# Performance work log

Hardware: AMD Instinct MI355X
Metric: run time of the kernel (lower is better)

Reference implementation:

```python
import jax, jax.numpy as jnp
import numpy as np

N = 1_000_000   # total atoms in batched graph
G = 50_000      # number of molecules (graphs)
F = 128         # gnn_out_feats (node feature dim)
H = 128         # classifier_hidden_feats
T = 12          # n_tasks
EPS = 1e-5      # BatchNorm1d eps


def setup_inputs() -> dict:
    key = jax.random.key(0)
    ks = jax.random.split(key, 20)
    s = 0.05
    inp = {}
    inp["node_feats"] = jax.random.normal(ks[0], (N, F), jnp.float32)
    inp["segment_ids"] = jnp.sort(jax.random.randint(ks[1], (N,), 0, G))
    inp["num_graphs"] = G
    # per-task atom weighting: Linear(F,1) per task, stacked -> [T,F]
    inp["atom_w"] = jax.random.normal(ks[2], (T, F), jnp.float32) * s
    inp["atom_b"] = jnp.zeros((T,), jnp.float32)
    # fc_layer 1: Linear(F,H) -> ReLU -> BatchNorm1d(H) (eval mode)
    inp["W1"] = jax.random.normal(ks[3], (T, F, H), jnp.float32) * s
    inp["b1"] = jnp.zeros((T, H), jnp.float32)
    inp["g1"] = jnp.ones((T, H), jnp.float32)
    inp["be1"] = jnp.zeros((T, H), jnp.float32)
    inp["rm1"] = jnp.zeros((T, H), jnp.float32)
    inp["rv1"] = jnp.ones((T, H), jnp.float32)
    # fc_layer 2 and 3: Linear(H,H) -> ReLU -> BatchNorm1d(H)
    inp["W2"] = jax.random.normal(ks[4], (T, H, H), jnp.float32) * s
    inp["b2"] = jnp.zeros((T, H), jnp.float32)
    inp["g2"] = jnp.ones((T, H), jnp.float32)
    inp["be2"] = jnp.zeros((T, H), jnp.float32)
    inp["rm2"] = jnp.zeros((T, H), jnp.float32)
    inp["rv2"] = jnp.ones((T, H), jnp.float32)
    inp["W3"] = jax.random.normal(ks[5], (T, H, H), jnp.float32) * s
    inp["b3"] = jnp.zeros((T, H), jnp.float32)
    inp["g3"] = jnp.ones((T, H), jnp.float32)
    inp["be3"] = jnp.zeros((T, H), jnp.float32)
    inp["rm3"] = jnp.zeros((T, H), jnp.float32)
    inp["rv3"] = jnp.ones((T, H), jnp.float32)
    # output_layer: Linear(H,H) -> ReLU -> Linear(H,1)
    inp["oW1"] = jax.random.normal(ks[6], (T, H, H), jnp.float32) * s
    inp["ob1"] = jnp.zeros((T, H), jnp.float32)
    inp["oW2"] = jax.random.normal(ks[7], (T, H), jnp.float32) * s
    inp["ob2"] = jnp.zeros((T,), jnp.float32)
    return inp


def _fc(x, W, b, g, be, rm, rv):
    # Linear -> ReLU -> BatchNorm1d (eval, running stats), batched over tasks t
    y = jax.nn.relu(jnp.einsum('gti,tio->gto', x, W) + b)
    return (y - rm) * (g * jax.lax.rsqrt(rv + EPS)) + be


def reference(node_feats, segment_ids, num_graphs, atom_w, atom_b,
              W1, b1, g1, be1, rm1, rv1,
              W2, b2, g2, be2, rm2, rv2,
              W3, b3, g3, be3, rm3, rv3,
              oW1, ob1, oW2, ob2):
    n_tasks = atom_w.shape[0]
    # WeightAndSum: per-task sigmoid node weights [N,T]
    w = jax.nn.sigmoid(node_feats @ atom_w.T + atom_b)
    # per-task weighted segment-sum pooling: loop over small fixed task count
    sums = [jax.ops.segment_sum(node_feats * w[:, t:t + 1], segment_ids,
                                num_segments=num_graphs)
            for t in range(n_tasks)]
    mol = jnp.stack(sums, axis=1)  # [G, T, F]
    h = _fc(mol, W1, b1, g1, be1, rm1, rv1)
    h = _fc(h, W2, b2, g2, be2, rm2, rv2)
    h = _fc(h, W3, b3, g3, be3, rm3, rv3)
    z = jax.nn.relu(jnp.einsum('gth,tho->gto', h, oW1) + ob1)
    pred = jnp.einsum('gth,th->gt', z, oW2) + ob2  # [G, T]
    return pred
```

## Files before the change

kernel.cpp:

```cpp
#include <hip/hip_runtime.h>
#include <hip/hip_bf16.h>
#include <hip/hip_fp16.h>

typedef _Float16 f16;
typedef _Float16 f16x2 __attribute__((ext_vector_type(2)));
typedef _Float16 f16x4 __attribute__((ext_vector_type(4)));
typedef _Float16 f16x8 __attribute__((ext_vector_type(8)));
typedef float f32x4 __attribute__((ext_vector_type(4)));

#define BN_EPS 1e-5f

__global__ void seg_starts_k(const int* __restrict__ seg, int N, int G, int* __restrict__ start) {
    int n = blockIdx.x * blockDim.x + threadIdx.x;
    if (n >= N) return;
    int s = seg[n];
    int p = (n == 0) ? -1 : seg[n - 1];
    for (int g = p + 1; g <= s; ++g) start[g] = n;
    if (n == N - 1) {
        for (int g = s + 1; g <= G; ++g) start[g] = N;
    }
}

__global__ void prep_k(const float* __restrict__ W1, const float* __restrict__ b1,
                       const float* __restrict__ W2, const float* __restrict__ b2,
                       const float* __restrict__ W3, const float* __restrict__ b3,
                       const float* __restrict__ oW1, const float* __restrict__ ob1,
                       const float* __restrict__ g1, const float* __restrict__ be1,
                       const float* __restrict__ rm1, const float* __restrict__ rv1,
                       const float* __restrict__ g2, const float* __restrict__ be2,
                       const float* __restrict__ rm2, const float* __restrict__ rv2,
                       const float* __restrict__ g3, const float* __restrict__ be3,
                       const float* __restrict__ rm3, const float* __restrict__ rv3,
                       f16* __restrict__ Wt, float* __restrict__ bp) {
    int T = gridDim.x;
    int t = blockIdx.x, l = blockIdx.y;
    int o = threadIdx.x;
    __shared__ float s_sh[128], c_sh[128];

    const float *W, *b, *gg = nullptr, *be = nullptr, *rm = nullptr, *rv = nullptr;
    if (l == 0)      { W = W1;  b = b1; }
    else if (l == 1) { W = W2;  b = b2;  gg = g1; be = be1; rm = rm1; rv = rv1; }
    else if (l == 2) { W = W3;  b = b3;  gg = g2; be = be2; rm = rm2; rv = rv2; }
    else             { W = oW1; b = ob1; gg = g3; be = be3; rm = rm3; rv = rv3; }

    float s = 1.f, c = 0.f;
    if (gg) {
        float sv = gg[t * 128 + o] * rsqrtf(rv[t * 128 + o] + BN_EPS);
        s = sv;
        c = be[t * 128 + o] - rm[t * 128 + o] * sv;
    }
    s_sh[o] = s;
    c_sh[o] = c;
    __syncthreads();

    const float* Wsrc = W + (size_t)t * 128 * 128;
    f16* Wdst = Wt + (((size_t)l * T + t) * 128 + o) * 128;
    float acc = b[t * 128 + o];
    for (int i = 0; i < 128; ++i) {
        float wv = Wsrc[i * 128 + o];
        Wdst[i] = (f16)(s_sh[i] * wv);
        acc += c_sh[i] * wv;
    }
    bp[((size_t)l * T + t) * 128 + o] = acc;
}

__global__ __launch_bounds__(256) void pool_k(const float* __restrict__ feats,
                                              const float* __restrict__ atom_w,
                                              const float* __restrict__ atom_b,
                                              const int* __restrict__ start,
                                              f16* __restrict__ mol, int G) {
    __shared__ f16 xs_all[4][2][16][128];

    int wave = threadIdx.x >> 6;
    int lane = threadIdx.x & 63;
    f16 (*xs)[16][128] = xs_all[wave];

    int g = blockIdx.x * 4 + wave;
    if (g >= G) return;

    int lr = lane & 15;
    int kg = lane >> 4;

    f16x8 bfr[4];
    float ab = 0.f;
#pragma unroll
    for (int ks = 0; ks < 4; ++ks) {
        f16x8 v = {};
        if (lr < 12) {
            const float* s = atom_w + lr * 128 + ks * 32 + kg * 8;
#pragma unroll
            for (int j = 0; j < 8; ++j) v[j] = (f16)s[j];
        }
        bfr[ks] = v;
    }
    if (lr < 12) ab = atom_b[lr];

    f32x4 acc[8];
#pragma unroll
    for (int nf = 0; nf < 8; ++nf) acc[nf] = (f32x4){0.f, 0.f, 0.f, 0.f};

    int a0 = start[g], a1 = start[g + 1];
    int nAtoms = a1 - a0;
    int nc = (nAtoms + 15) >> 4;

    float4 u[8];
    if (nc > 0) {
        int cn = nAtoms < 16 ? nAtoms : 16;
#pragma unroll
        for (int it = 0; it < 8; ++it) {
            int c = (it << 6) + lane;
            int r = c >> 5, q = c & 31;
            float4 v = make_float4(0.f, 0.f, 0.f, 0.f);
            if (r < cn) v = *(const float4*)(feats + (size_t)(a0 + r) * 128 + (q << 2));
            u[it] = v;
        }
    }

    for (int ci = 0; ci < nc; ++ci) {
        int cur = ci & 1;
#pragma unroll
        for (int it = 0; it < 8; ++it) {
            int c = (it << 6) + lane;
            int r = c >> 5, q = c & 31;
            f16x4 h;
            h[0] = (f16)u[it].x; h[1] = (f16)u[it].y;
            h[2] = (f16)u[it].z; h[3] = (f16)u[it].w;
            *(f16x4*)(&xs[cur][r][(((q >> 1) ^ (r & 7)) << 3) + ((q & 1) << 2)]) = h;
        }
        if (ci + 1 < nc) {
            int c0 = a0 + (ci + 1) * 16;
            int cn2 = a1 - c0; if (cn2 > 16) cn2 = 16;
#pragma unroll
            for (int it = 0; it < 8; ++it) {
                int c = (it << 6) + lane;
                int r = c >> 5, q = c & 31;
                float4 v = make_float4(0.f, 0.f, 0.f, 0.f);
                if (r < cn2) v = *(const float4*)(feats + (size_t)(c0 + r) * 128 + (q << 2));
                u[it] = v;
            }
        }
        int cn = nAtoms - ci * 16; if (cn > 16) cn = 16;

        f32x4 pa = {0.f, 0.f, 0.f, 0.f};
#pragma unroll
        for (int ks = 0; ks < 4; ++ks) {
            f16x8 afr = *(const f16x8*)(&xs[cur][lr][((((ks << 2) + kg)) ^ (lr & 7)) << 3]);
            pa = __builtin_amdgcn_mfma_f32_16x16x32_f16(afr, bfr[ks], pa, 0, 0, 0);
        }
        f16x4 a2;
#pragma unroll
        for (int j = 0; j < 4; ++j) {
            float w = 1.f / (1.f + __expf(-(pa[j] + ab)));
            int atom = (kg << 2) + j;
            a2[j] = (atom < cn) ? (f16)w : (f16)0.f;
        }
#pragma unroll
        for (int nf = 0; nf < 8; ++nf) {
            f16x4 b2;
#pragma unroll
            for (int j = 0; j < 4; ++j) {
                int a = (kg << 2) + j;
                int f = (nf << 4) + lr;
                b2[j] = xs[cur][a][(((f >> 3) ^ (a & 7)) << 3) + (f & 7)];
            }
            acc[nf] = __builtin_amdgcn_mfma_f32_16x16x16f16(a2, b2, acc[nf], 0, 0, 0);
        }
    }

    f16* dst = mol + (size_t)g * 12 * 128;
    if (kg < 3) {
#pragma unroll
        for (int nf = 0; nf < 8; ++nf) {
#pragma unroll
            for (int j = 0; j < 4; ++j) {
                dst[((kg << 2) + j) * 128 + (nf << 4) + lr] = (f16)acc[nf][j];
            }
        }
    }
}

__global__ __launch_bounds__(256, 2) void fc_k(const f16* __restrict__ mol,
                                               const f16* __restrict__ Wt,
                                               const float* __restrict__ bp,
                                               const float* __restrict__ oW2,
                                               const float* __restrict__ ob2,
                                               float* __restrict__ out, int G, int T) {
    __shared__ f16 A[2][64][128];
    __shared__ f16 B[128][128];

    int t = blockIdx.y;
    int g0 = blockIdx.x * 64;
    int tid = threadIdx.x;

    {
#pragma unroll
        for (int k = 0; k < 4; ++k) {
            int c = tid + k * 256;
            int r = c >> 4, sl = c & 15;
            uint4 v = make_uint4(0u, 0u, 0u, 0u);
            if (g0 + r < G)
                v = *(const uint4*)(mol + ((size_t)(g0 + r) * T + t) * 128 + sl * 8);
            *(uint4*)(&A[0][r][(sl ^ (r & 7)) * 8]) = v;
        }
    }
    {
        const f16* src = Wt + ((size_t)0 * T + t) * 128 * 128;
#pragma unroll
        for (int k = 0; k < 8; ++k) {
            int c = tid + k * 256;
            int r = c >> 4, sl = c & 15;
            uint4 v = *(const uint4*)(src + (size_t)r * 128 + sl * 8);
            *(uint4*)(&B[r][(sl ^ (r & 7)) * 8]) = v;
        }
    }
    __syncthreads();

    int wid = tid >> 6, lane = tid & 63;
    int lg = lane >> 4, lr = lane & 15;
    int m0 = wid * 16;
    int arow = m0 + lr;
    float pred[4] = {0.f, 0.f, 0.f, 0.f};
    int cur = 0;

    for (int l = 0; l < 4; ++l) {
        f16x8 afr[4];
#pragma unroll
        for (int ks = 0; ks < 4; ++ks) {
            int sl = (4 * ks + lg) ^ (arow & 7);
            afr[ks] = *(const f16x8*)(&A[cur][arow][sl * 8]);
        }
        const float* bias = bp + ((size_t)l * T + t) * 128;
#pragma unroll
        for (int nf = 0; nf < 8; ++nf) {
            int n = nf * 16 + lr;
            f32x4 acc = {0.f, 0.f, 0.f, 0.f};
#pragma unroll
            for (int ks = 0; ks < 4; ++ks) {
                int sl = (4 * ks + lg) ^ (n & 7);
                f16x8 bfr = *(const f16x8*)(&B[n][sl * 8]);
                acc = __builtin_amdgcn_mfma_f32_16x16x32_f16(afr[ks], bfr, acc, 0, 0, 0);
            }
            float bv = bias[n];
            if (l < 3) {
#pragma unroll
                for (int j = 0; j < 4; ++j) {
                    float y = acc[j] + bv;
                    y = y > 0.f ? y : 0.f;
                    int rr = m0 + 4 * lg + j;
                    A[cur ^ 1][rr][(((n >> 3) ^ (rr & 7)) << 3) + (n & 7)] = (f16)y;
                }
            } else {
                float w2 = oW2[t * 128 + n];
#pragma unroll
                for (int j = 0; j < 4; ++j) {
                    float z = acc[j] + bv;
                    z = z > 0.f ? z : 0.f;
                    pred[j] += z * w2;
                }
            }
        }
        __syncthreads();
        if (l < 3) {
            const f16* src = Wt + ((size_t)(l + 1) * T + t) * 128 * 128;
#pragma unroll
            for (int k = 0; k < 8; ++k) {
                int c = tid + k * 256;
                int r = c >> 4, sl = c & 15;
                uint4 v = *(const uint4*)(src + (size_t)r * 128 + sl * 8);
                *(uint4*)(&B[r][(sl ^ (r & 7)) * 8]) = v;
            }
            __syncthreads();
            cur ^= 1;
        }
    }

#pragma unroll
    for (int m = 1; m < 16; m <<= 1) {
#pragma unroll
        for (int j = 0; j < 4; ++j) pred[j] += __shfl_xor(pred[j], m, 64);
    }
    if (lr == 0) {
        float ob = ob2[t];
#pragma unroll
        for (int j = 0; j < 4; ++j) {
            int gg = g0 + m0 + 4 * lg + j;
            if (gg < G) out[(size_t)gg * T + t] = pred[j] + ob;
        }
    }
}

extern "C" void kernel_launch(void* const* d_in, const int* in_sizes, int n_in,
                              void* d_out, int out_size, void* d_ws, size_t ws_size,
                              hipStream_t stream) {
    const float* node_feats = (const float*)d_in[0];
    const int*   seg        = (const int*)d_in[1];
    const float* atom_w     = (const float*)d_in[3];
    const float* atom_b     = (const float*)d_in[4];
    const float* W1  = (const float*)d_in[5];
    const float* b1  = (const float*)d_in[6];
    const float* g1  = (const float*)d_in[7];
    const float* be1 = (const float*)d_in[8];
    const float* rm1 = (const float*)d_in[9];
    const float* rv1 = (const float*)d_in[10];
    const float* W2  = (const float*)d_in[11];
    const float* b2  = (const float*)d_in[12];
    const float* g2  = (const float*)d_in[13];
    const float* be2 = (const float*)d_in[14];
    const float* rm2 = (const float*)d_in[15];
    const float* rv2 = (const float*)d_in[16];
    const float* W3  = (const float*)d_in[17];
    const float* b3  = (const float*)d_in[18];
    const float* g3  = (const float*)d_in[19];
    const float* be3 = (const float*)d_in[20];
    const float* rm3 = (const float*)d_in[21];
    const float* rv3 = (const float*)d_in[22];
    const float* oW1 = (const float*)d_in[23];
    const float* ob1 = (const float*)d_in[24];
    const float* oW2 = (const float*)d_in[25];
    const float* ob2 = (const float*)d_in[26];

    int T = in_sizes[4];
    int F = in_sizes[3] / T;
    int N = in_sizes[0] / F;
    int G = out_size / T;

    char* ws = (char*)d_ws;
    size_t off = 0;
    int* start = (int*)ws;
    off += (((size_t)(G + 1) * 4) + 255) & ~(size_t)255;
    f16* Wt = (f16*)(ws + off);
    off += (((size_t)4 * T * 128 * 128 * 2) + 255) & ~(size_t)255;
    float* bp = (float*)(ws + off);
    off += (((size_t)4 * T * 128 * 4) + 255) & ~(size_t)255;
    f16* mol = (f16*)(ws + off);

    seg_starts_k<<<(N + 255) / 256, 256, 0, stream>>>(seg, N, G, start);
    prep_k<<<dim3(T, 4), 128, 0, stream>>>(W1, b1, W2, b2, W3, b3, oW1, ob1,
                                           g1, be1, rm1, rv1,
                                           g2, be2, rm2, rv2,
                                           g3, be3, rm3, rv3, Wt, bp);
    pool_k<<<(G + 3) / 4, 256, 0, stream>>>(node_feats, atom_w, atom_b, start, mol, G);
    fc_k<<<dim3((G + 63) / 64, T), 256, 0, stream>>>(mol, Wt, bp, oW2, ob2,
                                                     (float*)d_out, G, T);
}
```

Baseline: 372.6 us.

## Pool over contiguous 128-atom tiles with boundary partials and fixup kernel

Replaces the per-graph, one-wave-per-molecule pooling with blocks that each own a contiguous tile of 128 atoms. Each block computes the sigmoid task weights for the whole tile once, then segment-sums every graph that overlaps the tile. Graphs cut at a tile boundary write fp32 partials to a workspace, and a new fixup kernel adds the two halves. This is meant to remove the padding waste of 16-atom chunks on small graphs and the load imbalance between graphs, and to make feature loads fully coalesced. The cost is an extra launch and partial-sum traffic, and the code assumes no graph spans more than two tiles.

Measured after the change: 424.0 us. 13.8% more time.

```diff
diff --git a/kernel.cpp b/kernel.cpp
--- a/kernel.cpp
+++ b/kernel.cpp
@@ -64,22 +64,27 @@
     bp[((size_t)l * T + t) * 128 + o] = acc;
 }
 
-__global__ __launch_bounds__(256) void pool_k(const float* __restrict__ feats,
-                                              const float* __restrict__ atom_w,
-                                              const float* __restrict__ atom_b,
-                                              const int* __restrict__ start,
-                                              f16* __restrict__ mol, int G) {
-    __shared__ f16 xs_all[4][2][16][128];
-
-    int wave = threadIdx.x >> 6;
-    int lane = threadIdx.x & 63;
-    f16 (*xs)[16][128] = xs_all[wave];
-
-    int g = blockIdx.x * 4 + wave;
-    if (g >= G) return;
-
-    int lr = lane & 15;
-    int kg = lane >> 4;
+__global__ __launch_bounds__(256) void pool2_k(const float* __restrict__ feats,
+                                               const float* __restrict__ atom_w,
+                                               const float* __restrict__ atom_b,
+                                               const int* __restrict__ seg,
+                                               const int* __restrict__ start,
+                                               f16* __restrict__ mol,
+                                               float* __restrict__ pt,
+                                               int N, int G) {
+    __shared__ f16 xs[128][128];
+    __shared__ f16 wls[128][20];
+
+    int b = blockIdx.x;
+    int A0 = b * 128;
+    int cnt = N - A0; if (cnt > 128) cnt = 128;
+    int tid = threadIdx.x;
+    int wave = tid >> 6, lane = tid & 63;
+    int lr = lane & 15, kg = lane >> 4;
+
+    int segPrev = (A0 > 0) ? seg[A0 - 1] : -1;
+    int segFirst = seg[A0];
+    int segLast = seg[A0 + cnt - 1];
 
     f16x8 bfr[4];
     float ab = 0.f;
@@ -95,87 +100,128 @@
     }
     if (lr < 12) ab = atom_b[lr];
 
-    f32x4 acc[8];
-#pragma unroll
-    for (int nf = 0; nf < 8; ++nf) acc[nf] = (f32x4){0.f, 0.f, 0.f, 0.f};
-
-    int a0 = start[g], a1 = start[g + 1];
-    int nAtoms = a1 - a0;
-    int nc = (nAtoms + 15) >> 4;
-
-    float4 u[8];
-    if (nc > 0) {
-        int cn = nAtoms < 16 ? nAtoms : 16;
-#pragma unroll
-        for (int it = 0; it < 8; ++it) {
-            int c = (it << 6) + lane;
-            int r = c >> 5, q = c & 31;
-            float4 v = make_float4(0.f, 0.f, 0.f, 0.f);
-            if (r < cn) v = *(const float4*)(feats + (size_t)(a0 + r) * 128 + (q << 2));
-            u[it] = v;
-        }
-    }
-
-    for (int ci = 0; ci < nc; ++ci) {
-        int cur = ci & 1;
-#pragma unroll
-        for (int it = 0; it < 8; ++it) {
-            int c = (it << 6) + lane;
-            int r = c >> 5, q = c & 31;
-            f16x4 h;
-            h[0] = (f16)u[it].x; h[1] = (f16)u[it].y;
-            h[2] = (f16)u[it].z; h[3] = (f16)u[it].w;
-            *(f16x4*)(&xs[cur][r][(((q >> 1) ^ (r & 7)) << 3) + ((q & 1) << 2)]) = h;
-        }
-        if (ci + 1 < nc) {
-            int c0 = a0 + (ci + 1) * 16;
-            int cn2 = a1 - c0; if (cn2 > 16) cn2 = 16;
-#pragma unroll
-            for (int it = 0; it < 8; ++it) {
-                int c = (it << 6) + lane;
-                int r = c >> 5, q = c & 31;
-                float4 v = make_float4(0.f, 0.f, 0.f, 0.f);
-                if (r < cn2) v = *(const float4*)(feats + (size_t)(c0 + r) * 128 + (q << 2));
-                u[it] = v;
+#pragma unroll
+    for (int it = 0; it < 16; ++it) {
+        int v = tid + it * 256;
+        int r = v >> 5, q = v & 31;
+        float4 u = make_float4(0.f, 0.f, 0.f, 0.f);
+        if (r < cnt) u = *(const float4*)(feats + (size_t)A0 * 128 + (size_t)v * 4);
+        f16x4 h;
+        h[0] = (f16)u.x; h[1] = (f16)u.y; h[2] = (f16)u.z; h[3] = (f16)u.w;
+        *(f16x4*)(&xs[r][(((q >> 1) ^ (r & 7)) << 3) + ((q & 1) << 2)]) = h;
+    }
+    __syncthreads();
+
+#pragma unroll
+    for (int tt = 0; tt < 2; ++tt) {
+        int tau = wave + tt * 4;
+        f32x4 pa = {0.f, 0.f, 0.f, 0.f};
+#pragma unroll
+        for (int ks = 0; ks < 4; ++ks) {
+            int row = tau * 16 + lr;
+            f16x8 afr = *(const f16x8*)(&xs[row][((((ks << 2) + kg)) ^ (lr & 7)) << 3]);
+            pa = __builtin_amdgcn_mfma_f32_16x16x32_f16(afr, bfr[ks], pa, 0, 0, 0);
+        }
+#pragma unroll
+        for (int j = 0; j < 4; ++j) {
+            float w = (lr < 12) ? 1.f / (1.f + __expf(-(pa[j] + ab))) : 0.f;
+            wls[tau * 16 + (kg << 2) + j][lr] = (f16)w;
+        }
+    }
+    __syncthreads();
+
+    int gA = (A0 == 0) ? 0 : segPrev + 1;
+    if (A0 > 0 && segFirst == segPrev) gA = segFirst;
+    int gHi = (A0 + cnt >= N) ? (G - 1) : segLast;
+
+    for (int g = gA + wave; g <= gHi; g += 4) {
+        int s = start[g], e = start[g + 1];
+        int lls = s - A0; if (lls < 0) lls = 0;
+        int lle = e - A0; if (lle > cnt) lle = cnt;
+
+        f32x4 acc[8];
+#pragma unroll
+        for (int nf = 0; nf < 8; ++nf) acc[nf] = (f32x4){0.f, 0.f, 0.f, 0.f};
+
+        if (lls < lle) {
+            int ta = lls >> 4, tb = (lle - 1) >> 4;
+            for (int tau = ta; tau <= tb; ++tau) {
+                f16x4 a2;
+#pragma unroll
+                for (int j = 0; j < 4; ++j) {
+                    int la = tau * 16 + (kg << 2) + j;
+                    f16 w = wls[la][lr];
+                    a2[j] = (la >= lls && la < lle) ? w : (f16)0.f;
+                }
+#pragma unroll
+                for (int nf = 0; nf < 8; ++nf) {
+                    f16x4 b2;
+#pragma unroll
+                    for (int j = 0; j < 4; ++j) {
+                        int la = tau * 16 + (kg << 2) + j;
+                        int f = (nf << 4) + lr;
+                        b2[j] = xs[la][(((f >> 3) ^ (la & 7)) << 3) + (f & 7)];
+                    }
+                    acc[nf] = __builtin_amdgcn_mfma_f32_16x16x16f16(a2, b2, acc[nf], 0, 0, 0);
+                }
             }
         }
-        int cn = nAtoms - ci * 16; if (cn > 16) cn = 16;
-
-        f32x4 pa = {0.f, 0.f, 0.f, 0.f};
-#pragma unroll
-        for (int ks = 0; ks < 4; ++ks) {
-            f16x8 afr = *(const f16x8*)(&xs[cur][lr][((((ks << 2) + kg)) ^ (lr & 7)) << 3]);
-            pa = __builtin_amdgcn_mfma_f32_16x16x32_f16(afr, bfr[ks], pa, 0, 0, 0);
-        }
-        f16x4 a2;
-#pragma unroll
-        for (int j = 0; j < 4; ++j) {
-            float w = 1.f / (1.f + __expf(-(pa[j] + ab)));
-            int atom = (kg << 2) + j;
-            a2[j] = (atom < cn) ? (f16)w : (f16)0.f;
-        }
-#pragma unroll
-        for (int nf = 0; nf < 8; ++nf) {
-            f16x4 b2;
-#pragma unroll
-            for (int j = 0; j < 4; ++j) {
-                int a = (kg << 2) + j;
-                int f = (nf << 4) + lr;
-                b2[j] = xs[cur][a][(((f >> 3) ^ (a & 7)) << 3) + (f & 7)];
-            }
-            acc[nf] = __builtin_amdgcn_mfma_f32_16x16x16f16(a2, b2, acc[nf], 0, 0, 0);
-        }
-    }
-
-    f16* dst = mol + (size_t)g * 12 * 128;
-    if (kg < 3) {
-#pragma unroll
-        for (int nf = 0; nf < 8; ++nf) {
-#pragma unroll
-            for (int j = 0; j < 4; ++j) {
-                dst[((kg << 2) + j) * 128 + (nf << 4) + lr] = (f16)acc[nf][j];
-            }
-        }
+
+        bool tailcut = (e > A0 + cnt) && (A0 + cnt < N);
+        bool headcut = (s < A0);
+        if (tailcut) {
+            float* d = pt + ((size_t)b * 2 + 0) * 1536;
+            if (kg < 3) {
+#pragma unroll
+                for (int nf = 0; nf < 8; ++nf)
+#pragma unroll
+                    for (int j = 0; j < 4; ++j)
+                        d[((kg << 2) + j) * 128 + (nf << 4) + lr] = acc[nf][j];
+        } } else if (headcut) {
+            float* d = pt + ((size_t)(b - 1) * 2 + 1) * 1536;
+            if (kg < 3) {
+#pragma unroll
+                for (int nf = 0; nf < 8; ++nf)
+#pragma unroll
+                    for (int j = 0; j < 4; ++j)
+                        d[((kg << 2) + j) * 128 + (nf << 4) + lr] = acc[nf][j];
+        } } else {
+            f16* d = mol + (size_t)g * 1536;
+            if (kg < 3) {
+#pragma unroll
+                for (int nf = 0; nf < 8; ++nf)
+#pragma unroll
+                    for (int j = 0; j < 4; ++j)
+                        d[((kg << 2) + j) * 128 + (nf << 4) + lr] = (f16)acc[nf][j];
+        } }
+    }
+}
+
+__global__ __launch_bounds__(256) void fixup_k(const int* __restrict__ seg,
+                                               const float* __restrict__ pt,
+                                               f16* __restrict__ mol, int nbd) {
+    int wave = threadIdx.x >> 6, lane = threadIdx.x & 63;
+    int bd = blockIdx.x * 4 + wave;
+    if (bd >= nbd) return;
+    int p = (bd + 1) * 128;
+    int g0 = seg[p - 1], g1 = seg[p];
+    if (g0 != g1) return;
+    const float* p0 = pt + (size_t)bd * 2 * 1536;
+    const float* p1 = p0 + 1536;
+    f16* d = mol + (size_t)g1 * 1536;
+#pragma unroll
+    for (int it = 0; it < 3; ++it) {
+        int i = it * 512 + lane * 8;
+        float4 a0 = *(const float4*)(p0 + i);
+        float4 a1 = *(const float4*)(p0 + i + 4);
+        float4 c0 = *(const float4*)(p1 + i);
+        float4 c1 = *(const float4*)(p1 + i + 4);
+        f16x8 h;
+        h[0] = (f16)(a0.x + c0.x); h[1] = (f16)(a0.y + c0.y);
+        h[2] = (f16)(a0.z + c0.z); h[3] = (f16)(a0.w + c0.w);
+        h[4] = (f16)(a1.x + c1.x); h[5] = (f16)(a1.y + c1.y);
+        h[6] = (f16)(a1.z + c1.z); h[7] = (f16)(a1.w + c1.w);
+        *(f16x8*)(d + i) = h;
     }
 }
 
@@ -323,6 +369,8 @@
     int F = in_sizes[3] / T;
     int N = in_sizes[0] / F;
     int G = out_size / T;
+    int nb = (N + 127) / 128;
+    int nbd = nb - 1;
 
     char* ws = (char*)d_ws;
     size_t off = 0;
@@ -333,13 +381,16 @@
     float* bp = (float*)(ws + off);
     off += (((size_t)4 * T * 128 * 4) + 255) & ~(size_t)255;
     f16* mol = (f16*)(ws + off);
+    off += (((size_t)G * 12 * 128 * 2) + 255) & ~(size_t)255;
+    float* pt = (float*)(ws + off);
 
     seg_starts_k<<<(N + 255) / 256, 256, 0, stream>>>(seg, N, G, start);
     prep_k<<<dim3(T, 4), 128, 0, stream>>>(W1, b1, W2, b2, W3, b3, oW1, ob1,
                                            g1, be1, rm1, rv1,
                                            g2, be2, rm2, rv2,
                                            g3, be3, rm3, rv3, Wt, bp);
-    pool_k<<<(G + 3) / 4, 256, 0, stream>>>(node_feats, atom_w, atom_b, start, mol, G);
+    pool2_k<<<nb, 256, 0, stream>>>(node_feats, atom_w, atom_b, seg, start, mol, pt, N, G);
+    fixup_k<<<(nbd + 3) / 4, 256, 0, stream>>>(seg, pt, mol, nbd);
     fc_k<<<dim3((G + 63) / 64, T), 256, 0, stream>>>(mol, Wt, bp, oW2, ob2,
                                                      (float*)d_out, G, T);
 }
```
